# Optimization experiments

Hardware: AMD Instinct MI355X
Metric: run time of the kernel (lower is better)

## Reference

```python
import jax, jax.numpy as jnp
import numpy as np

N, DIM, EDGE_DIM, HEADS, EXP_HEADS, E = 50000, 64, 32, 8, 16, 800000
HEAD_DIM = DIM // HEADS
SCALE = HEAD_DIM ** -0.5
EPS = 1e-16


def setup_inputs() -> dict:
    key = jax.random.key(0)
    ks = jax.random.split(key, 16)
    s = DIM ** -0.5
    return {
        "x": jax.random.normal(ks[0], (N, DIM), jnp.float32),
        "edges": jax.random.normal(ks[1], (E, EDGE_DIM), jnp.float32),
        "edge_index": jax.random.randint(ks[2], (2, E), 0, N, jnp.int64),
        "Wq": jax.random.normal(ks[3], (DIM, DIM), jnp.float32) * s,
        "Wk": jax.random.normal(ks[4], (DIM, DIM), jnp.float32) * s,
        "Wv": jax.random.normal(ks[5], (DIM, DIM), jnp.float32) * s,
        "Wek": jax.random.normal(ks[6], (EDGE_DIM, DIM), jnp.float32) * (EDGE_DIM ** -0.5),
        "Wev": jax.random.normal(ks[7], (EDGE_DIM, DIM), jnp.float32) * (EDGE_DIM ** -0.5),
        "Wexp": jax.random.normal(ks[8], (HEADS, EXP_HEADS), jnp.float32) * (HEADS ** -0.5),
        "Wsq": jax.random.normal(ks[9], (EXP_HEADS, HEADS), jnp.float32) * (EXP_HEADS ** -0.5),
        "bsq": jax.random.normal(ks[10], (HEADS,), jnp.float32) * 0.01,
        "Wout": jax.random.normal(ks[11], (DIM, DIM), jnp.float32) * s,
        "bout": jax.random.normal(ks[12], (DIM,), jnp.float32) * 0.01,
        "temperature": jnp.full((1,), 0.01, jnp.float32),
    }


def reference(x, edges, edge_index, Wq, Wk, Wv, Wek, Wev, Wexp, Wsq, bsq, Wout, bout, temperature):
    n = x.shape[0]
    dst = edge_index[0]  # segment / query index
    src = edge_index[1]  # key/value gather index

    q = (x @ Wq).reshape(n, HEADS, HEAD_DIM)      # [n,h,d]
    k = (x @ Wk).reshape(n, HEADS, HEAD_DIM)
    v = (x @ Wv).reshape(n, HEADS, HEAD_DIM)      # v_non_scatter

    qe = q[dst]                                   # [E,h,d] edge gathers
    ke = k[src]
    ve = v[src]

    edge_k = (edges @ Wek).reshape(-1, HEADS, HEAD_DIM)
    edge_v = (edges @ Wev).reshape(-1, HEADS, HEAD_DIM)

    ke = (ke + edge_k) * SCALE
    attn = jnp.einsum('ehd,ehd->eh', qe, ke) / temperature[0]  # [E,h]
    attn = attn @ Wexp                                          # [E,eh]

    # sparse (segment) softmax over edges grouped by dst, per expanded head
    mx = jax.ops.segment_max(attn, dst, num_segments=n)         # [n,eh]
    ex = jnp.exp(attn - mx[dst])
    sm = jax.ops.segment_sum(ex, dst, num_segments=n)
    attn = ex / (sm[dst] + EPS)

    attn = attn @ Wsq + bsq                                     # [E,h]

    ve = ve + edge_v
    out_e = attn[:, :, None] * ve                               # [E,h,d]
    agg = jax.ops.segment_sum(out_e, dst, num_segments=n)       # [n,h,d]

    out = (v - agg).reshape(n, DIM)                             # graph Laplacian: v - aggregated
    out = out @ Wout + bout
    return out, attn.T  # attention returned as [h, E]
```

## Files before the change

kernel.cpp:

```cpp
#include <hip/hip_runtime.h>
#include <hip/hip_fp16.h>

#define N_NODES 50000
#define DIM 64
#define EDGE_DIM 32
#define HEADS 8
#define EXP_HEADS 16
#define NEDGE 800000
#define SCALE 0.35355339059327373f
#define EPS 1e-16f
#define NEG_BIG -1e30f
#define NB_SCAN ((N_NODES + 255) / 256)

#define RFL(x) __builtin_amdgcn_readfirstlane(x)

__device__ __forceinline__ float h2f(unsigned short u) {
    __half h;
    *reinterpret_cast<unsigned short*>(&h) = u;
    return __half2float(h);
}
__device__ __forceinline__ unsigned short f2h(float f) {
    __half h = __float2half(f);
    return *reinterpret_cast<unsigned short*>(&h);
}

__global__ __launch_bounds__(256) void qkv_kernel(
    const float* __restrict__ x, const float* __restrict__ Wq,
    const float* __restrict__ Wk, const float* __restrict__ Wv,
    float* __restrict__ q, float* __restrict__ k, float* __restrict__ v,
    unsigned short* __restrict__ vh) {
    int gid = blockIdx.x * 256 + threadIdx.x;
    if (gid >= (N_NODES / 4) * DIM) return;
    int quad = gid >> 6, j = gid & 63;
    long i0 = (long)quad * 4;
    float aq[4] = {0,0,0,0}, ak[4] = {0,0,0,0}, av[4] = {0,0,0,0};
#pragma unroll
    for (int l = 0; l < DIM; ++l) {
        float wq = Wq[l * DIM + j], wk = Wk[l * DIM + j], wv = Wv[l * DIM + j];
#pragma unroll
        for (int r = 0; r < 4; ++r) {
            float xv = x[(i0 + r) * DIM + l];
            aq[r] = fmaf(xv, wq, aq[r]);
            ak[r] = fmaf(xv, wk, ak[r]);
            av[r] = fmaf(xv, wv, av[r]);
        }
    }
#pragma unroll
    for (int r = 0; r < 4; ++r) {
        q[(i0 + r) * DIM + j] = aq[r];
        k[(i0 + r) * DIM + j] = ak[r];
        v[(i0 + r) * DIM + j] = av[r];
        vh[(i0 + r) * DIM + j] = f2h(av[r]);
    }
}

__global__ __launch_bounds__(256) void hist_kernel(
    const int* __restrict__ eidx, unsigned* __restrict__ cnt) {
    int e = blockIdx.x * 256 + threadIdx.x;
    if (e >= NEDGE) return;
    atomicAdd(&cnt[eidx[e]], 1u);
}

__global__ __launch_bounds__(256) void scan_reduce(
    const unsigned* __restrict__ cnt, unsigned* __restrict__ blocksum) {
    int gid = blockIdx.x * 256 + threadIdx.x;
    unsigned v = (gid < N_NODES) ? cnt[gid] : 0u;
    v += __shfl_xor(v, 1);  v += __shfl_xor(v, 2);
    v += __shfl_xor(v, 4);  v += __shfl_xor(v, 8);
    v += __shfl_xor(v, 16); v += __shfl_xor(v, 32);
    __shared__ unsigned ws4[4];
    if ((threadIdx.x & 63) == 0) ws4[threadIdx.x >> 6] = v;
    __syncthreads();
    if (threadIdx.x == 0)
        blocksum[blockIdx.x] = ws4[0] + ws4[1] + ws4[2] + ws4[3];
}

__global__ __launch_bounds__(256) void scan_base(
    const unsigned* __restrict__ blocksum, unsigned* __restrict__ blockbase) {
    __shared__ unsigned ps[256];
    int t = threadIdx.x;
    unsigned v = (t < NB_SCAN) ? blocksum[t] : 0u;
    ps[t] = v;
    __syncthreads();
    for (int off = 1; off < 256; off <<= 1) {
        unsigned val = (t >= off) ? ps[t - off] : 0u;
        __syncthreads();
        ps[t] += val;
        __syncthreads();
    }
    blockbase[t] = ps[t] - v;
}

__global__ __launch_bounds__(256) void scan_final(
    const unsigned* __restrict__ cnt, const unsigned* __restrict__ blockbase,
    unsigned* __restrict__ offsets, unsigned* __restrict__ cursor) {
    __shared__ unsigned ps[256];
    int t = threadIdx.x;
    int gid = blockIdx.x * 256 + t;
    unsigned v = (gid < N_NODES) ? cnt[gid] : 0u;
    ps[t] = v;
    __syncthreads();
    for (int off = 1; off < 256; off <<= 1) {
        unsigned val = (t >= off) ? ps[t - off] : 0u;
        __syncthreads();
        ps[t] += val;
        __syncthreads();
    }
    unsigned off_ = blockbase[blockIdx.x] + ps[t] - v;
    if (gid < N_NODES) { offsets[gid] = off_; cursor[gid] = off_; }
    if (gid == N_NODES - 1) offsets[N_NODES] = off_ + v;
}

__global__ __launch_bounds__(256) void scatter_kernel(
    const int* __restrict__ eidx, unsigned* __restrict__ cursor,
    unsigned* __restrict__ perm, unsigned* __restrict__ iperm,
    unsigned* __restrict__ srcs) {
    int e = blockIdx.x * 256 + threadIdx.x;
    if (e >= NEDGE) return;
    int dst = eidx[e];
    unsigned pos = atomicAdd(&cursor[dst], 1u);
    perm[pos] = e;
    iperm[e] = pos;
    srcs[pos] = (unsigned)eidx[NEDGE + e];
}

#define HALVE_BLOCKS 2048
__global__ __launch_bounds__(256) void halve_kernel(
    const float4* __restrict__ src, ushort4* __restrict__ dst) {
    const long n4 = (long)NEDGE * EDGE_DIM / 4;
    long i = (long)blockIdx.x * 256 + threadIdx.x;
    const long stride = (long)HALVE_BLOCKS * 256;
    for (; i < n4; i += stride) {
        float4 t = src[i];
        ushort4 o;
        o.x = f2h(t.x); o.y = f2h(t.y); o.z = f2h(t.z); o.w = f2h(t.w);
        dst[i] = o;
    }
}

__global__ __launch_bounds__(256) void edge_attn_kernel(
    const float* __restrict__ edges,
    const float* __restrict__ q, const float* __restrict__ k,
    const float* __restrict__ Wek,
    const float* __restrict__ temp, const unsigned* __restrict__ perm,
    const unsigned* __restrict__ offsets, const unsigned* __restrict__ srcs,
    float* __restrict__ logit8) {
    int tid = threadIdx.x;
    int w = tid >> 6, lane = tid & 63;
    int h = lane >> 3, d = lane & 7;
    float wekr[4][8];
#pragma unroll
    for (int j = 0; j < 4; ++j)
#pragma unroll
        for (int i = 0; i < 8; ++i)
            wekr[j][i] = Wek[(d * 4 + j) * DIM + h * 8 + i];
    float invt = SCALE / temp[0];
    int n = blockIdx.x * 4 + w;
    unsigned nb = offsets[n];
    int deg = (int)(offsets[n + 1] - nb);
    const float* __restrict__ qp = q + (long)n * DIM;
    float qreg = qp[lane];
    float qv[8];
#pragma unroll
    for (int t = 0; t < 8; ++t) qv[t] = qp[h * 8 + t];
    float g0 = 0.f, g1 = 0.f, g2 = 0.f, g3 = 0.f;
#pragma unroll
    for (int t = 0; t < 8; ++t) {
        g0 = fmaf(qv[t], wekr[0][t], g0);
        g1 = fmaf(qv[t], wekr[1][t], g1);
        g2 = fmaf(qv[t], wekr[2][t], g2);
        g3 = fmaf(qv[t], wekr[3][t], g3);
    }
    int j = 0;
    for (; j + 4 <= deg; j += 4) {
        float p[4];
#pragma unroll
        for (int g2i = 0; g2i < 4; ++g2i) {
            long slot = (long)nb + j + g2i;
            int e_g = RFL((int)perm[slot]);
            int s_g = RFL((int)srcs[slot]);
            float kv = k[(long)s_g * DIM + lane];
            float4 ed = *(const float4*)(edges + (long)e_g * EDGE_DIM + d * 4);
            float pp = qreg * kv;
            pp = fmaf(g0, ed.x, pp);
            pp = fmaf(g1, ed.y, pp);
            pp = fmaf(g2, ed.z, pp);
            pp = fmaf(g3, ed.w, pp);
            p[g2i] = pp;
        }
#pragma unroll
        for (int i = 0; i < 4; ++i) p[i] += __shfl_xor(p[i], 1);
#pragma unroll
        for (int i = 0; i < 4; ++i) p[i] += __shfl_xor(p[i], 2);
#pragma unroll
        for (int i = 0; i < 4; ++i) p[i] += __shfl_xor(p[i], 4);
        if (d == 0) {
#pragma unroll
            for (int i = 0; i < 4; ++i)
                logit8[((long)nb + j + i) * HEADS + h] = p[i] * invt;
        }
    }
    for (; j < deg; ++j) {
        long slot = (long)nb + j;
        int e_g = RFL((int)perm[slot]);
        int s_g = RFL((int)srcs[slot]);
        float kv = k[(long)s_g * DIM + lane];
        float4 ed = *(const float4*)(edges + (long)e_g * EDGE_DIM + d * 4);
        float pp = qreg * kv;
        pp = fmaf(g0, ed.x, pp);
        pp = fmaf(g1, ed.y, pp);
        pp = fmaf(g2, ed.z, pp);
        pp = fmaf(g3, ed.w, pp);
        pp += __shfl_xor(pp, 1);
        pp += __shfl_xor(pp, 2);
        pp += __shfl_xor(pp, 4);
        if (d == 0) logit8[slot * HEADS + h] = pp * invt;
    }
}

__global__ __launch_bounds__(256) void node_fused_kernel(
    const unsigned short* __restrict__ ehalf,
    const unsigned short* __restrict__ vh,
    const float* __restrict__ v, const float* __restrict__ logit8,
    const unsigned* __restrict__ offsets, const unsigned* __restrict__ perm,
    const unsigned* __restrict__ srcs,
    const float* __restrict__ Wexp, const float* __restrict__ Wsq,
    const float* __restrict__ bsq, const float* __restrict__ Wev,
    float* __restrict__ a8s, float* __restrict__ vmagg) {
    int tid = threadIdx.x;
    int w = tid >> 6, lane = tid & 63;
    int g = lane >> 4, t16 = lane & 15;
    int h = lane >> 3, d = lane & 7;
    float we[HEADS];
#pragma unroll
    for (int hh = 0; hh < HEADS; ++hh) we[hh] = Wexp[hh * EXP_HEADS + t16];
    float wsq[HEADS];
#pragma unroll
    for (int j = 0; j < HEADS; ++j) wsq[j] = Wsq[t16 * HEADS + j];
    int hmap = 4 * (t16 & 1) + 2 * ((t16 >> 1) & 1) + ((t16 >> 2) & 1);
    int ih = ((h >> 2) & 1) | (((h >> 1) & 1) << 1) | ((h & 1) << 2);
    float bs_h = bsq[h], bs_w = bsq[hmap];
    bool b0 = (t16 & 1), b1 = (t16 & 2), b2 = (t16 & 4);

    int n = blockIdx.x * 4 + w;
    unsigned nb = offsets[n];
    int deg = (int)(offsets[n + 1] - nb);

    float m = NEG_BIG, s = 0.f;
    for (int j0 = 0; j0 < deg; j0 += 4) {
        const float4* lp = (const float4*)(logit8 + ((long)nb + j0 + g) * HEADS);
        float4 l0 = lp[0], l1 = lp[1];
        float a = l0.x * we[0];
        a = fmaf(l0.y, we[1], a); a = fmaf(l0.z, we[2], a); a = fmaf(l0.w, we[3], a);
        a = fmaf(l1.x, we[4], a); a = fmaf(l1.y, we[5], a);
        a = fmaf(l1.z, we[6], a); a = fmaf(l1.w, we[7], a);
        if (j0 + g < deg) {
            float mn = fmaxf(m, a);
            s = s * __expf(m - mn) + __expf(a - mn);
            m = mn;
        }
    }
#pragma unroll
    for (int off = 16; off < 64; off <<= 1) {
        float m2 = __shfl_xor(m, off), s2 = __shfl_xor(s, off);
        float mn = fmaxf(m, m2);
        s = s * __expf(m - mn) + s2 * __expf(m2 - mn);
        m = mn;
    }
    float rs = 1.f / (s + EPS);

    float acc = 0.f, t0 = 0.f, t1 = 0.f, t2 = 0.f, t3 = 0.f;
    for (int j0 = 0; j0 < deg; j0 += 4) {
        int cnt = deg - j0; if (cnt > 4) cnt = 4;
        const float4* lp = (const float4*)(logit8 + ((long)nb + j0 + g) * HEADS);
        float4 l0 = lp[0], l1 = lp[1];
        float a = l0.x * we[0];
        a = fmaf(l0.y, we[1], a); a = fmaf(l0.z, we[2], a); a = fmaf(l0.w, we[3], a);
        a = fmaf(l1.x, we[4], a); a = fmaf(l1.y, we[5], a);
        a = fmaf(l1.z, we[6], a); a = fmaf(l1.w, we[7], a);
        float p = (g < cnt) ? __expf(a - m) * rs : 0.f;
        float v0 = p * wsq[0], v1 = p * wsq[1], v2 = p * wsq[2], v3 = p * wsq[3];
        float v4 = p * wsq[4], v5 = p * wsq[5], v6 = p * wsq[6], v7 = p * wsq[7];
        float q0, q1, q2, q3, n0, n1, s8;
        q0 = (b0 ? v4 : v0) + __shfl_xor(b0 ? v0 : v4, 1);
        q1 = (b0 ? v5 : v1) + __shfl_xor(b0 ? v1 : v5, 1);
        q2 = (b0 ? v6 : v2) + __shfl_xor(b0 ? v2 : v6, 1);
        q3 = (b0 ? v7 : v3) + __shfl_xor(b0 ? v3 : v7, 1);
        n0 = (b1 ? q2 : q0) + __shfl_xor(b1 ? q0 : q2, 2);
        n1 = (b1 ? q3 : q1) + __shfl_xor(b1 ? q1 : q3, 2);
        s8 = (b2 ? n1 : n0) + __shfl_xor(b2 ? n0 : n1, 4);
        float a8sum = s8 + __shfl_xor(s8, 8);
        if (t16 < 8 && g < cnt)
            a8s[((long)nb + j0 + g) * HEADS + hmap] = a8sum + bs_w;
#pragma unroll
        for (int i = 0; i < 4; ++i) {
            if (i < cnt) {
                long slot = (long)nb + j0 + i;
                int e_g = RFL((int)perm[slot]);
                int s_g = RFL((int)srcs[slot]);
                float a8 = __shfl(a8sum, i * 16 + ih) + bs_h;
                float vv = h2f(vh[(long)s_g * DIM + lane]);
                ushort4 ue = *(const ushort4*)(ehalf + (long)e_g * EDGE_DIM + d * 4);
                acc = fmaf(a8, vv, acc);
                t0 = fmaf(a8, h2f(ue.x), t0);
                t1 = fmaf(a8, h2f(ue.y), t1);
                t2 = fmaf(a8, h2f(ue.z), t2);
                t3 = fmaf(a8, h2f(ue.w), t3);
            }
        }
    }
    float ev = 0.f;
#pragma unroll
    for (int l = 0; l < EDGE_DIM; ++l) {
        float tv = ((l & 3) == 0) ? t0 : ((l & 3) == 1) ? t1 : ((l & 3) == 2) ? t2 : t3;
        float tl = __shfl(tv, h * 8 + (l >> 2));
        ev = fmaf(tl, Wev[l * DIM + lane], ev);
    }
    vmagg[(long)n * DIM + lane] = v[(long)n * DIM + lane] - (acc + ev);
}

__global__ __launch_bounds__(256) void transpose_kernel(
    const float* __restrict__ a8s, const unsigned* __restrict__ iperm,
    float* __restrict__ out2) {
    int e = blockIdx.x * 256 + threadIdx.x;
    if (e >= NEDGE) return;
    long sj = iperm[e];
    const float4* p = (const float4*)(a8s + sj * HEADS);
    float4 lo = p[0], hi = p[1];
    out2[0L * NEDGE + e] = lo.x; out2[1L * NEDGE + e] = lo.y;
    out2[2L * NEDGE + e] = lo.z; out2[3L * NEDGE + e] = lo.w;
    out2[4L * NEDGE + e] = hi.x; out2[5L * NEDGE + e] = hi.y;
    out2[6L * NEDGE + e] = hi.z; out2[7L * NEDGE + e] = hi.w;
}

__global__ __launch_bounds__(256) void out_kernel(
    const float* __restrict__ vmagg, const float* __restrict__ Wout,
    const float* __restrict__ bout, float* __restrict__ out) {
    int gid = blockIdx.x * 256 + threadIdx.x;
    if (gid >= (N_NODES / 4) * DIM) return;
    int quad = gid >> 6, j = gid & 63;
    long i0 = (long)quad * 4;
    float b = bout[j];
    float ac[4] = {b, b, b, b};
#pragma unroll
    for (int l = 0; l < DIM; ++l) {
        float wv = Wout[l * DIM + j];
#pragma unroll
        for (int r = 0; r < 4; ++r)
            ac[r] = fmaf(vmagg[(i0 + r) * DIM + l], wv, ac[r]);
    }
#pragma unroll
    for (int r = 0; r < 4; ++r) out[(i0 + r) * DIM + j] = ac[r];
}

extern "C" void kernel_launch(void* const* d_in, const int* in_sizes, int n_in,
                              void* d_out, int out_size, void* d_ws, size_t ws_size,
                              hipStream_t stream) {
    const float* x     = (const float*)d_in[0];
    const float* edges = (const float*)d_in[1];
    const int*   eidx  = (const int*)d_in[2];
    const float* Wq    = (const float*)d_in[3];
    const float* Wk    = (const float*)d_in[4];
    const float* Wv    = (const float*)d_in[5];
    const float* Wek   = (const float*)d_in[6];
    const float* Wev   = (const float*)d_in[7];
    const float* Wexp  = (const float*)d_in[8];
    const float* Wsq   = (const float*)d_in[9];
    const float* bsq   = (const float*)d_in[10];
    const float* Wout  = (const float*)d_in[11];
    const float* bout  = (const float*)d_in[12];
    const float* temp  = (const float*)d_in[13];

    float* ws = (float*)d_ws;
    float* q       = ws;
    float* k       = ws + 3200000L;
    float* v       = ws + 6400000L;
    float* logit8  = ws + 9600000L;
    float* vmagg   = ws + 16000000L;
    float* a8s     = q;
    unsigned* perm      = (unsigned*)(ws + 19200000L);
    unsigned* iperm     = perm + NEDGE;
    unsigned* srcs      = iperm + NEDGE;
    unsigned* cnt       = srcs + NEDGE;
    unsigned* offsets   = cnt + N_NODES;
    unsigned* cursor    = offsets + N_NODES + 1;
    unsigned* blocksum  = cursor + N_NODES;
    unsigned* blockbase = blocksum + 256;
    unsigned short* ehalf = (unsigned short*)(ws + 21800000L);
    unsigned short* vh    = (unsigned short*)(ws + 34600000L);

    hipMemsetAsync(cnt, 0, (size_t)N_NODES * sizeof(unsigned), stream);

    float* out1 = (float*)d_out;
    float* out2 = out1 + (long)N_NODES * DIM;

    qkv_kernel<<<(N_NODES / 4 * DIM + 255) / 256, 256, 0, stream>>>(x, Wq, Wk, Wv, q, k, v, vh);
    hist_kernel<<<(NEDGE + 255) / 256, 256, 0, stream>>>(eidx, cnt);
    scan_reduce<<<NB_SCAN, 256, 0, stream>>>(cnt, blocksum);
    scan_base<<<1, 256, 0, stream>>>(blocksum, blockbase);
    scan_final<<<NB_SCAN, 256, 0, stream>>>(cnt, blockbase, offsets, cursor);
    halve_kernel<<<HALVE_BLOCKS, 256, 0, stream>>>((const float4*)edges, (ushort4*)ehalf);
    scatter_kernel<<<(NEDGE + 255) / 256, 256, 0, stream>>>(eidx, cursor, perm, iperm, srcs);
    edge_attn_kernel<<<N_NODES / 4, 256, 0, stream>>>(edges, q, k, Wek, temp,
                                                      perm, offsets, srcs, logit8);
    node_fused_kernel<<<N_NODES / 4, 256, 0, stream>>>(ehalf, vh, v, logit8, offsets, perm, srcs,
                                                       Wexp, Wsq, bsq, Wev, a8s, vmagg);
    transpose_kernel<<<(NEDGE + 255) / 256, 256, 0, stream>>>(a8s, iperm, out2);
    out_kernel<<<(N_NODES / 4 * DIM + 255) / 256, 256, 0, stream>>>(vmagg, Wout, bout, out1);
}
```

Before: 466.4 us.

## Read fp16 keys and edges in edge attention; unroll node softmax loops by eight

```diff
diff --git a/kernel.cpp b/kernel.cpp
--- a/kernel.cpp
+++ b/kernel.cpp
@@ -27,8 +27,8 @@
 __global__ __launch_bounds__(256) void qkv_kernel(
     const float* __restrict__ x, const float* __restrict__ Wq,
     const float* __restrict__ Wk, const float* __restrict__ Wv,
-    float* __restrict__ q, float* __restrict__ k, float* __restrict__ v,
-    unsigned short* __restrict__ vh) {
+    float* __restrict__ q, unsigned short* __restrict__ kh,
+    float* __restrict__ v, unsigned short* __restrict__ vh) {
     int gid = blockIdx.x * 256 + threadIdx.x;
     if (gid >= (N_NODES / 4) * DIM) return;
     int quad = gid >> 6, j = gid & 63;
@@ -48,7 +48,7 @@
 #pragma unroll
     for (int r = 0; r < 4; ++r) {
         q[(i0 + r) * DIM + j] = aq[r];
-        k[(i0 + r) * DIM + j] = ak[r];
+        kh[(i0 + r) * DIM + j] = f2h(ak[r]);
         v[(i0 + r) * DIM + j] = av[r];
         vh[(i0 + r) * DIM + j] = f2h(av[r]);
     }
@@ -139,8 +139,8 @@
 }
 
 __global__ __launch_bounds__(256) void edge_attn_kernel(
-    const float* __restrict__ edges,
-    const float* __restrict__ q, const float* __restrict__ k,
+    const unsigned short* __restrict__ ehalf,
+    const float* __restrict__ q, const unsigned short* __restrict__ kh,
     const float* __restrict__ Wek,
     const float* __restrict__ temp, const unsigned* __restrict__ perm,
     const unsigned* __restrict__ offsets, const unsigned* __restrict__ srcs,
@@ -179,13 +179,13 @@
             long slot = (long)nb + j + g2i;
             int e_g = RFL((int)perm[slot]);
             int s_g = RFL((int)srcs[slot]);
-            float kv = k[(long)s_g * DIM + lane];
-            float4 ed = *(const float4*)(edges + (long)e_g * EDGE_DIM + d * 4);
+            float kv = h2f(kh[(long)s_g * DIM + lane]);
+            ushort4 ue = *(const ushort4*)(ehalf + (long)e_g * EDGE_DIM + d * 4);
             float pp = qreg * kv;
-            pp = fmaf(g0, ed.x, pp);
-            pp = fmaf(g1, ed.y, pp);
-            pp = fmaf(g2, ed.z, pp);
-            pp = fmaf(g3, ed.w, pp);
+            pp = fmaf(g0, h2f(ue.x), pp);
+            pp = fmaf(g1, h2f(ue.y), pp);
+            pp = fmaf(g2, h2f(ue.z), pp);
+            pp = fmaf(g3, h2f(ue.w), pp);
             p[g2i] = pp;
         }
 #pragma unroll
@@ -204,13 +204,13 @@
         long slot = (long)nb + j;
         int e_g = RFL((int)perm[slot]);
         int s_g = RFL((int)srcs[slot]);
-        float kv = k[(long)s_g * DIM + lane];
-        float4 ed = *(const float4*)(edges + (long)e_g * EDGE_DIM + d * 4);
+        float kv = h2f(kh[(long)s_g * DIM + lane]);
+        ushort4 ue = *(const ushort4*)(ehalf + (long)e_g * EDGE_DIM + d * 4);
         float pp = qreg * kv;
-        pp = fmaf(g0, ed.x, pp);
-        pp = fmaf(g1, ed.y, pp);
-        pp = fmaf(g2, ed.z, pp);
-        pp = fmaf(g3, ed.w, pp);
+        pp = fmaf(g0, h2f(ue.x), pp);
+        pp = fmaf(g1, h2f(ue.y), pp);
+        pp = fmaf(g2, h2f(ue.z), pp);
+        pp = fmaf(g3, h2f(ue.w), pp);
         pp += __shfl_xor(pp, 1);
         pp += __shfl_xor(pp, 2);
         pp += __shfl_xor(pp, 4);
@@ -246,8 +246,28 @@
     unsigned nb = offsets[n];
     int deg = (int)(offsets[n + 1] - nb);
 
-    float m = NEG_BIG, s = 0.f;
-    for (int j0 = 0; j0 < deg; j0 += 4) {
+    float ma = NEG_BIG, sa = 0.f, mb = NEG_BIG, sb = 0.f;
+    int j0 = 0;
+    for (; j0 + 8 <= deg; j0 += 8) {
+        const float4* lpA = (const float4*)(logit8 + ((long)nb + j0 + g) * HEADS);
+        const float4* lpB = (const float4*)(logit8 + ((long)nb + j0 + 4 + g) * HEADS);
+        float4 a0 = lpA[0], a1 = lpA[1], c0 = lpB[0], c1 = lpB[1];
+        float aA = a0.x * we[0];
+        float aB = c0.x * we[0];
+        aA = fmaf(a0.y, we[1], aA); aB = fmaf(c0.y, we[1], aB);
+        aA = fmaf(a0.z, we[2], aA); aB = fmaf(c0.z, we[2], aB);
+        aA = fmaf(a0.w, we[3], aA); aB = fmaf(c0.w, we[3], aB);
+        aA = fmaf(a1.x, we[4], aA); aB = fmaf(c1.x, we[4], aB);
+        aA = fmaf(a1.y, we[5], aA); aB = fmaf(c1.y, we[5], aB);
+        aA = fmaf(a1.z, we[6], aA); aB = fmaf(c1.z, we[6], aB);
+        aA = fmaf(a1.w, we[7], aA); aB = fmaf(c1.w, we[7], aB);
+        float mnA = fmaxf(ma, aA);
+        float mnB = fmaxf(mb, aB);
+        sa = sa * __expf(ma - mnA) + __expf(aA - mnA);
+        sb = sb * __expf(mb - mnB) + __expf(aB - mnB);
+        ma = mnA; mb = mnB;
+    }
+    for (; j0 < deg; j0 += 4) {
         const float4* lp = (const float4*)(logit8 + ((long)nb + j0 + g) * HEADS);
         float4 l0 = lp[0], l1 = lp[1];
         float a = l0.x * we[0];
@@ -255,11 +275,17 @@
         a = fmaf(l1.x, we[4], a); a = fmaf(l1.y, we[5], a);
         a = fmaf(l1.z, we[6], a); a = fmaf(l1.w, we[7], a);
         if (j0 + g < deg) {
-            float mn = fmaxf(m, a);
-            s = s * __expf(m - mn) + __expf(a - mn);
-            m = mn;
-        }
-    }
+            float mn = fmaxf(ma, a);
+            sa = sa * __expf(ma - mn) + __expf(a - mn);
+            ma = mn;
+        }
+    }
+    {
+        float mn = fmaxf(ma, mb);
+        sa = sa * __expf(ma - mn) + sb * __expf(mb - mn);
+        ma = mn;
+    }
+    float m = ma, s = sa;
 #pragma unroll
     for (int off = 16; off < 64; off <<= 1) {
         float m2 = __shfl_xor(m, off), s2 = __shfl_xor(s, off);
@@ -270,7 +296,78 @@
     float rs = 1.f / (s + EPS);
 
     float acc = 0.f, t0 = 0.f, t1 = 0.f, t2 = 0.f, t3 = 0.f;
-    for (int j0 = 0; j0 < deg; j0 += 4) {
+    j0 = 0;
+    for (; j0 + 8 <= deg; j0 += 8) {
+        const float4* lpA = (const float4*)(logit8 + ((long)nb + j0 + g) * HEADS);
+        const float4* lpB = (const float4*)(logit8 + ((long)nb + j0 + 4 + g) * HEADS);
+        float4 a0 = lpA[0], a1 = lpA[1], c0 = lpB[0], c1 = lpB[1];
+        float aA = a0.x * we[0];
+        float aB = c0.x * we[0];
+        aA = fmaf(a0.y, we[1], aA); aB = fmaf(c0.y, we[1], aB);
+        aA = fmaf(a0.z, we[2], aA); aB = fmaf(c0.z, we[2], aB);
+        aA = fmaf(a0.w, we[3], aA); aB = fmaf(c0.w, we[3], aB);
+        aA = fmaf(a1.x, we[4], aA); aB = fmaf(c1.x, we[4], aB);
+        aA = fmaf(a1.y, we[5], aA); aB = fmaf(c1.y, we[5], aB);
+        aA = fmaf(a1.z, we[6], aA); aB = fmaf(c1.z, we[6], aB);
+        aA = fmaf(a1.w, we[7], aA); aB = fmaf(c1.w, we[7], aB);
+        float pA = __expf(aA - m) * rs;
+        float pB = __expf(aB - m) * rs;
+        float vA0 = pA * wsq[0], vA1 = pA * wsq[1], vA2 = pA * wsq[2], vA3 = pA * wsq[3];
+        float vA4 = pA * wsq[4], vA5 = pA * wsq[5], vA6 = pA * wsq[6], vA7 = pA * wsq[7];
+        float vB0 = pB * wsq[0], vB1 = pB * wsq[1], vB2 = pB * wsq[2], vB3 = pB * wsq[3];
+        float vB4 = pB * wsq[4], vB5 = pB * wsq[5], vB6 = pB * wsq[6], vB7 = pB * wsq[7];
+        float qA0, qA1, qA2, qA3, nA0, nA1, sA8;
+        float qB0, qB1, qB2, qB3, nB0, nB1, sB8;
+        qA0 = (b0 ? vA4 : vA0) + __shfl_xor(b0 ? vA0 : vA4, 1);
+        qB0 = (b0 ? vB4 : vB0) + __shfl_xor(b0 ? vB0 : vB4, 1);
+        qA1 = (b0 ? vA5 : vA1) + __shfl_xor(b0 ? vA1 : vA5, 1);
+        qB1 = (b0 ? vB5 : vB1) + __shfl_xor(b0 ? vB1 : vB5, 1);
+        qA2 = (b0 ? vA6 : vA2) + __shfl_xor(b0 ? vA2 : vA6, 1);
+        qB2 = (b0 ? vB6 : vB2) + __shfl_xor(b0 ? vB2 : vB6, 1);
+        qA3 = (b0 ? vA7 : vA3) + __shfl_xor(b0 ? vA3 : vA7, 1);
+        qB3 = (b0 ? vB7 : vB3) + __shfl_xor(b0 ? vB3 : vB7, 1);
+        nA0 = (b1 ? qA2 : qA0) + __shfl_xor(b1 ? qA0 : qA2, 2);
+        nB0 = (b1 ? qB2 : qB0) + __shfl_xor(b1 ? qB0 : qB2, 2);
+        nA1 = (b1 ? qA3 : qA1) + __shfl_xor(b1 ? qA1 : qA3, 2);
+        nB1 = (b1 ? qB3 : qB1) + __shfl_xor(b1 ? qB1 : qB3, 2);
+        sA8 = (b2 ? nA1 : nA0) + __shfl_xor(b2 ? nA0 : nA1, 4);
+        sB8 = (b2 ? nB1 : nB0) + __shfl_xor(b2 ? nB0 : nB1, 4);
+        float a8sumA = sA8 + __shfl_xor(sA8, 8);
+        float a8sumB = sB8 + __shfl_xor(sB8, 8);
+        if (t16 < 8) {
+            a8s[((long)nb + j0 + g) * HEADS + hmap] = a8sumA + bs_w;
+            a8s[((long)nb + j0 + 4 + g) * HEADS + hmap] = a8sumB + bs_w;
+        }
+#pragma unroll
+        for (int i = 0; i < 4; ++i) {
+            long slot = (long)nb + j0 + i;
+            int e_g = RFL((int)perm[slot]);
+            int s_g = RFL((int)srcs[slot]);
+            float a8 = __shfl(a8sumA, i * 16 + ih) + bs_h;
+            float vv = h2f(vh[(long)s_g * DIM + lane]);
+            ushort4 ue = *(const ushort4*)(ehalf + (long)e_g * EDGE_DIM + d * 4);
+            acc = fmaf(a8, vv, acc);
+            t0 = fmaf(a8, h2f(ue.x), t0);
+            t1 = fmaf(a8, h2f(ue.y), t1);
+            t2 = fmaf(a8, h2f(ue.z), t2);
+            t3 = fmaf(a8, h2f(ue.w), t3);
+        }
+#pragma unroll
+        for (int i = 0; i < 4; ++i) {
+            long slot = (long)nb + j0 + 4 + i;
+            int e_g = RFL((int)perm[slot]);
+            int s_g = RFL((int)srcs[slot]);
+            float a8 = __shfl(a8sumB, i * 16 + ih) + bs_h;
+            float vv = h2f(vh[(long)s_g * DIM + lane]);
+            ushort4 ue = *(const ushort4*)(ehalf + (long)e_g * EDGE_DIM + d * 4);
+            acc = fmaf(a8, vv, acc);
+            t0 = fmaf(a8, h2f(ue.x), t0);
+            t1 = fmaf(a8, h2f(ue.y), t1);
+            t2 = fmaf(a8, h2f(ue.z), t2);
+            t3 = fmaf(a8, h2f(ue.w), t3);
+        }
+    }
+    for (; j0 < deg; j0 += 4) {
         int cnt = deg - j0; if (cnt > 4) cnt = 4;
         const float4* lp = (const float4*)(logit8 + ((long)nb + j0 + g) * HEADS);
         float4 l0 = lp[0], l1 = lp[1];
@@ -373,7 +470,7 @@
 
     float* ws = (float*)d_ws;
     float* q       = ws;
-    float* k       = ws + 3200000L;
+    unsigned short* kh = (unsigned short*)(ws + 3200000L);
     float* v       = ws + 6400000L;
     float* logit8  = ws + 9600000L;
     float* vmagg   = ws + 16000000L;
@@ -394,14 +491,14 @@
     float* out1 = (float*)d_out;
     float* out2 = out1 + (long)N_NODES * DIM;
 
-    qkv_kernel<<<(N_NODES / 4 * DIM + 255) / 256, 256, 0, stream>>>(x, Wq, Wk, Wv, q, k, v, vh);
+    qkv_kernel<<<(N_NODES / 4 * DIM + 255) / 256, 256, 0, stream>>>(x, Wq, Wk, Wv, q, kh, v, vh);
     hist_kernel<<<(NEDGE + 255) / 256, 256, 0, stream>>>(eidx, cnt);
     scan_reduce<<<NB_SCAN, 256, 0, stream>>>(cnt, blocksum);
     scan_base<<<1, 256, 0, stream>>>(blocksum, blockbase);
     scan_final<<<NB_SCAN, 256, 0, stream>>>(cnt, blockbase, offsets, cursor);
     halve_kernel<<<HALVE_BLOCKS, 256, 0, stream>>>((const float4*)edges, (ushort4*)ehalf);
     scatter_kernel<<<(NEDGE + 255) / 256, 256, 0, stream>>>(eidx, cursor, perm, iperm, srcs);
-    edge_attn_kernel<<<N_NODES / 4, 256, 0, stream>>>(edges, q, k, Wek, temp,
+    edge_attn_kernel<<<N_NODES / 4, 256, 0, stream>>>(ehalf, q, kh, Wek, temp,
                                                       perm, offsets, srcs, logit8);
     node_fused_kernel<<<N_NODES / 4, 256, 0, stream>>>(ehalf, vh, v, logit8, offsets, perm, srcs,
                                                        Wexp, Wsq, bsq, Wev, a8s, vmagg);
```

New measurement: 460.9 us. Within noise of the previous version (-1.2%).

## Use fp16 keys and edges in attention kernel and batch gathers ahead of math

Applied to the files above, without the earlier changes.

```diff
diff --git a/kernel.cpp b/kernel.cpp
--- a/kernel.cpp
+++ b/kernel.cpp
@@ -27,8 +27,8 @@
 __global__ __launch_bounds__(256) void qkv_kernel(
     const float* __restrict__ x, const float* __restrict__ Wq,
     const float* __restrict__ Wk, const float* __restrict__ Wv,
-    float* __restrict__ q, float* __restrict__ k, float* __restrict__ v,
-    unsigned short* __restrict__ vh) {
+    float* __restrict__ q, unsigned short* __restrict__ kh,
+    float* __restrict__ v, unsigned short* __restrict__ vh) {
     int gid = blockIdx.x * 256 + threadIdx.x;
     if (gid >= (N_NODES / 4) * DIM) return;
     int quad = gid >> 6, j = gid & 63;
@@ -48,7 +48,7 @@
 #pragma unroll
     for (int r = 0; r < 4; ++r) {
         q[(i0 + r) * DIM + j] = aq[r];
-        k[(i0 + r) * DIM + j] = ak[r];
+        kh[(i0 + r) * DIM + j] = f2h(ak[r]);
         v[(i0 + r) * DIM + j] = av[r];
         vh[(i0 + r) * DIM + j] = f2h(av[r]);
     }
@@ -139,8 +139,8 @@
 }
 
 __global__ __launch_bounds__(256) void edge_attn_kernel(
-    const float* __restrict__ edges,
-    const float* __restrict__ q, const float* __restrict__ k,
+    const unsigned short* __restrict__ ehalf,
+    const float* __restrict__ q, const unsigned short* __restrict__ kh,
     const float* __restrict__ Wek,
     const float* __restrict__ temp, const unsigned* __restrict__ perm,
     const unsigned* __restrict__ offsets, const unsigned* __restrict__ srcs,
@@ -173,20 +173,24 @@
     }
     int j = 0;
     for (; j + 4 <= deg; j += 4) {
-        float p[4];
-#pragma unroll
-        for (int g2i = 0; g2i < 4; ++g2i) {
-            long slot = (long)nb + j + g2i;
+        unsigned short rk[4]; ushort4 re[4];
+#pragma unroll
+        for (int i = 0; i < 4; ++i) {
+            long slot = (long)nb + j + i;
             int e_g = RFL((int)perm[slot]);
             int s_g = RFL((int)srcs[slot]);
-            float kv = k[(long)s_g * DIM + lane];
-            float4 ed = *(const float4*)(edges + (long)e_g * EDGE_DIM + d * 4);
-            float pp = qreg * kv;
-            pp = fmaf(g0, ed.x, pp);
-            pp = fmaf(g1, ed.y, pp);
-            pp = fmaf(g2, ed.z, pp);
-            pp = fmaf(g3, ed.w, pp);
-            p[g2i] = pp;
+            rk[i] = kh[(long)s_g * DIM + lane];
+            re[i] = *(const ushort4*)(ehalf + (long)e_g * EDGE_DIM + d * 4);
+        }
+        float p[4];
+#pragma unroll
+        for (int i = 0; i < 4; ++i) {
+            float pp = qreg * h2f(rk[i]);
+            pp = fmaf(g0, h2f(re[i].x), pp);
+            pp = fmaf(g1, h2f(re[i].y), pp);
+            pp = fmaf(g2, h2f(re[i].z), pp);
+            pp = fmaf(g3, h2f(re[i].w), pp);
+            p[i] = pp;
         }
 #pragma unroll
         for (int i = 0; i < 4; ++i) p[i] += __shfl_xor(p[i], 1);
@@ -204,13 +208,13 @@
         long slot = (long)nb + j;
         int e_g = RFL((int)perm[slot]);
         int s_g = RFL((int)srcs[slot]);
-        float kv = k[(long)s_g * DIM + lane];
-        float4 ed = *(const float4*)(edges + (long)e_g * EDGE_DIM + d * 4);
+        float kv = h2f(kh[(long)s_g * DIM + lane]);
+        ushort4 ue = *(const ushort4*)(ehalf + (long)e_g * EDGE_DIM + d * 4);
         float pp = qreg * kv;
-        pp = fmaf(g0, ed.x, pp);
-        pp = fmaf(g1, ed.y, pp);
-        pp = fmaf(g2, ed.z, pp);
-        pp = fmaf(g3, ed.w, pp);
+        pp = fmaf(g0, h2f(ue.x), pp);
+        pp = fmaf(g1, h2f(ue.y), pp);
+        pp = fmaf(g2, h2f(ue.z), pp);
+        pp = fmaf(g3, h2f(ue.w), pp);
         pp += __shfl_xor(pp, 1);
         pp += __shfl_xor(pp, 2);
         pp += __shfl_xor(pp, 4);
@@ -269,11 +273,22 @@
     }
     float rs = 1.f / (s + EPS);
 
-    float acc = 0.f, t0 = 0.f, t1 = 0.f, t2 = 0.f, t3 = 0.f;
+    float accA = 0.f, accB = 0.f, t0 = 0.f, t1 = 0.f, t2 = 0.f, t3 = 0.f;
     for (int j0 = 0; j0 < deg; j0 += 4) {
         int cnt = deg - j0; if (cnt > 4) cnt = 4;
         const float4* lp = (const float4*)(logit8 + ((long)nb + j0 + g) * HEADS);
         float4 l0 = lp[0], l1 = lp[1];
+        unsigned short rv[4]; ushort4 re[4];
+#pragma unroll
+        for (int i = 0; i < 4; ++i) {
+            if (i < cnt) {
+                long slot = (long)nb + j0 + i;
+                int e_g = RFL((int)perm[slot]);
+                int s_g = RFL((int)srcs[slot]);
+                rv[i] = vh[(long)s_g * DIM + lane];
+                re[i] = *(const ushort4*)(ehalf + (long)e_g * EDGE_DIM + d * 4);
+            }
+        }
         float a = l0.x * we[0];
         a = fmaf(l0.y, we[1], a); a = fmaf(l0.z, we[2], a); a = fmaf(l0.w, we[3], a);
         a = fmaf(l1.x, we[4], a); a = fmaf(l1.y, we[5], a);
@@ -295,20 +310,18 @@
 #pragma unroll
         for (int i = 0; i < 4; ++i) {
             if (i < cnt) {
-                long slot = (long)nb + j0 + i;
-                int e_g = RFL((int)perm[slot]);
-                int s_g = RFL((int)srcs[slot]);
                 float a8 = __shfl(a8sum, i * 16 + ih) + bs_h;
-                float vv = h2f(vh[(long)s_g * DIM + lane]);
-                ushort4 ue = *(const ushort4*)(ehalf + (long)e_g * EDGE_DIM + d * 4);
-                acc = fmaf(a8, vv, acc);
-                t0 = fmaf(a8, h2f(ue.x), t0);
-                t1 = fmaf(a8, h2f(ue.y), t1);
-                t2 = fmaf(a8, h2f(ue.z), t2);
-                t3 = fmaf(a8, h2f(ue.w), t3);
+                float vv = h2f(rv[i]);
+                if (i & 1) accB = fmaf(a8, vv, accB);
+                else       accA = fmaf(a8, vv, accA);
+                t0 = fmaf(a8, h2f(re[i].x), t0);
+                t1 = fmaf(a8, h2f(re[i].y), t1);
+                t2 = fmaf(a8, h2f(re[i].z), t2);
+                t3 = fmaf(a8, h2f(re[i].w), t3);
             }
         }
     }
+    float acc = accA + accB;
     float ev = 0.f;
 #pragma unroll
     for (int l = 0; l < EDGE_DIM; ++l) {
@@ -373,7 +386,7 @@
 
     float* ws = (float*)d_ws;
     float* q       = ws;
-    float* k       = ws + 3200000L;
+    unsigned short* kh = (unsigned short*)(ws + 3200000L);
     float* v       = ws + 6400000L;
     float* logit8  = ws + 9600000L;
     float* vmagg   = ws + 16000000L;
@@ -394,14 +407,14 @@
     float* out1 = (float*)d_out;
     float* out2 = out1 + (long)N_NODES * DIM;
 
-    qkv_kernel<<<(N_NODES / 4 * DIM + 255) / 256, 256, 0, stream>>>(x, Wq, Wk, Wv, q, k, v, vh);
+    qkv_kernel<<<(N_NODES / 4 * DIM + 255) / 256, 256, 0, stream>>>(x, Wq, Wk, Wv, q, kh, v, vh);
     hist_kernel<<<(NEDGE + 255) / 256, 256, 0, stream>>>(eidx, cnt);
     scan_reduce<<<NB_SCAN, 256, 0, stream>>>(cnt, blocksum);
     scan_base<<<1, 256, 0, stream>>>(blocksum, blockbase);
     scan_final<<<NB_SCAN, 256, 0, stream>>>(cnt, blockbase, offsets, cursor);
     halve_kernel<<<HALVE_BLOCKS, 256, 0, stream>>>((const float4*)edges, (ushort4*)ehalf);
     scatter_kernel<<<(NEDGE + 255) / 256, 256, 0, stream>>>(eidx, cursor, perm, iperm, srcs);
-    edge_attn_kernel<<<N_NODES / 4, 256, 0, stream>>>(edges, q, k, Wek, temp,
+    edge_attn_kernel<<<N_NODES / 4, 256, 0, stream>>>(ehalf, q, kh, Wek, temp,
                                                       perm, offsets, srcs, logit8);
     node_fused_kernel<<<N_NODES / 4, 256, 0, stream>>>(ehalf, vh, v, logit8, offsets, perm, srcs,
                                                        Wexp, Wsq, bsq, Wev, a8s, vmagg);
```

Measured after the change: 486.1 us. +4.2%, slower.

## Pre-permute edge features into dst-sorted fp16 layout during scatter; store k as fp16

Applied to the files above, without the earlier changes.

```diff
diff --git a/kernel.cpp b/kernel.cpp
--- a/kernel.cpp
+++ b/kernel.cpp
@@ -27,8 +27,8 @@
 __global__ __launch_bounds__(256) void qkv_kernel(
     const float* __restrict__ x, const float* __restrict__ Wq,
     const float* __restrict__ Wk, const float* __restrict__ Wv,
-    float* __restrict__ q, float* __restrict__ k, float* __restrict__ v,
-    unsigned short* __restrict__ vh) {
+    float* __restrict__ q, unsigned short* __restrict__ kh,
+    float* __restrict__ v, unsigned short* __restrict__ vh) {
     int gid = blockIdx.x * 256 + threadIdx.x;
     if (gid >= (N_NODES / 4) * DIM) return;
     int quad = gid >> 6, j = gid & 63;
@@ -48,7 +48,7 @@
 #pragma unroll
     for (int r = 0; r < 4; ++r) {
         q[(i0 + r) * DIM + j] = aq[r];
-        k[(i0 + r) * DIM + j] = ak[r];
+        kh[(i0 + r) * DIM + j] = f2h(ak[r]);
         v[(i0 + r) * DIM + j] = av[r];
         vh[(i0 + r) * DIM + j] = f2h(av[r]);
     }
@@ -112,37 +112,32 @@
 }
 
 __global__ __launch_bounds__(256) void scatter_kernel(
-    const int* __restrict__ eidx, unsigned* __restrict__ cursor,
-    unsigned* __restrict__ perm, unsigned* __restrict__ iperm,
-    unsigned* __restrict__ srcs) {
+    const int* __restrict__ eidx, const float4* __restrict__ edges4,
+    unsigned* __restrict__ cursor,
+    unsigned* __restrict__ iperm, unsigned* __restrict__ srcs,
+    unsigned short* __restrict__ esort) {
     int e = blockIdx.x * 256 + threadIdx.x;
     if (e >= NEDGE) return;
     int dst = eidx[e];
     unsigned pos = atomicAdd(&cursor[dst], 1u);
-    perm[pos] = e;
     iperm[e] = pos;
     srcs[pos] = (unsigned)eidx[NEDGE + e];
-}
-
-#define HALVE_BLOCKS 2048
-__global__ __launch_bounds__(256) void halve_kernel(
-    const float4* __restrict__ src, ushort4* __restrict__ dst) {
-    const long n4 = (long)NEDGE * EDGE_DIM / 4;
-    long i = (long)blockIdx.x * 256 + threadIdx.x;
-    const long stride = (long)HALVE_BLOCKS * 256;
-    for (; i < n4; i += stride) {
+    const float4* src = edges4 + (long)e * 8;
+    ushort4* dst4 = (ushort4*)(esort + (long)pos * EDGE_DIM);
+#pragma unroll
+    for (int i = 0; i < 8; ++i) {
         float4 t = src[i];
         ushort4 o;
         o.x = f2h(t.x); o.y = f2h(t.y); o.z = f2h(t.z); o.w = f2h(t.w);
-        dst[i] = o;
+        dst4[i] = o;
     }
 }
 
 __global__ __launch_bounds__(256) void edge_attn_kernel(
-    const float* __restrict__ edges,
-    const float* __restrict__ q, const float* __restrict__ k,
+    const unsigned short* __restrict__ esort,
+    const float* __restrict__ q, const unsigned short* __restrict__ kh,
     const float* __restrict__ Wek,
-    const float* __restrict__ temp, const unsigned* __restrict__ perm,
+    const float* __restrict__ temp,
     const unsigned* __restrict__ offsets, const unsigned* __restrict__ srcs,
     float* __restrict__ logit8) {
     int tid = threadIdx.x;
@@ -177,15 +172,14 @@
 #pragma unroll
         for (int g2i = 0; g2i < 4; ++g2i) {
             long slot = (long)nb + j + g2i;
-            int e_g = RFL((int)perm[slot]);
             int s_g = RFL((int)srcs[slot]);
-            float kv = k[(long)s_g * DIM + lane];
-            float4 ed = *(const float4*)(edges + (long)e_g * EDGE_DIM + d * 4);
+            float kv = h2f(kh[(long)s_g * DIM + lane]);
+            ushort4 ue = *(const ushort4*)(esort + slot * EDGE_DIM + d * 4);
             float pp = qreg * kv;
-            pp = fmaf(g0, ed.x, pp);
-            pp = fmaf(g1, ed.y, pp);
-            pp = fmaf(g2, ed.z, pp);
-            pp = fmaf(g3, ed.w, pp);
+            pp = fmaf(g0, h2f(ue.x), pp);
+            pp = fmaf(g1, h2f(ue.y), pp);
+            pp = fmaf(g2, h2f(ue.z), pp);
+            pp = fmaf(g3, h2f(ue.w), pp);
             p[g2i] = pp;
         }
 #pragma unroll
@@ -202,15 +196,14 @@
     }
     for (; j < deg; ++j) {
         long slot = (long)nb + j;
-        int e_g = RFL((int)perm[slot]);
         int s_g = RFL((int)srcs[slot]);
-        float kv = k[(long)s_g * DIM + lane];
-        float4 ed = *(const float4*)(edges + (long)e_g * EDGE_DIM + d * 4);
+        float kv = h2f(kh[(long)s_g * DIM + lane]);
+        ushort4 ue = *(const ushort4*)(esort + slot * EDGE_DIM + d * 4);
         float pp = qreg * kv;
-        pp = fmaf(g0, ed.x, pp);
-        pp = fmaf(g1, ed.y, pp);
-        pp = fmaf(g2, ed.z, pp);
-        pp = fmaf(g3, ed.w, pp);
+        pp = fmaf(g0, h2f(ue.x), pp);
+        pp = fmaf(g1, h2f(ue.y), pp);
+        pp = fmaf(g2, h2f(ue.z), pp);
+        pp = fmaf(g3, h2f(ue.w), pp);
         pp += __shfl_xor(pp, 1);
         pp += __shfl_xor(pp, 2);
         pp += __shfl_xor(pp, 4);
@@ -219,10 +212,10 @@
 }
 
 __global__ __launch_bounds__(256) void node_fused_kernel(
-    const unsigned short* __restrict__ ehalf,
+    const unsigned short* __restrict__ esort,
     const unsigned short* __restrict__ vh,
     const float* __restrict__ v, const float* __restrict__ logit8,
-    const unsigned* __restrict__ offsets, const unsigned* __restrict__ perm,
+    const unsigned* __restrict__ offsets,
     const unsigned* __restrict__ srcs,
     const float* __restrict__ Wexp, const float* __restrict__ Wsq,
     const float* __restrict__ bsq, const float* __restrict__ Wev,
@@ -296,11 +289,10 @@
         for (int i = 0; i < 4; ++i) {
             if (i < cnt) {
                 long slot = (long)nb + j0 + i;
-                int e_g = RFL((int)perm[slot]);
                 int s_g = RFL((int)srcs[slot]);
                 float a8 = __shfl(a8sum, i * 16 + ih) + bs_h;
                 float vv = h2f(vh[(long)s_g * DIM + lane]);
-                ushort4 ue = *(const ushort4*)(ehalf + (long)e_g * EDGE_DIM + d * 4);
+                ushort4 ue = *(const ushort4*)(esort + slot * EDGE_DIM + d * 4);
                 acc = fmaf(a8, vv, acc);
                 t0 = fmaf(a8, h2f(ue.x), t0);
                 t1 = fmaf(a8, h2f(ue.y), t1);
@@ -373,20 +365,19 @@
 
     float* ws = (float*)d_ws;
     float* q       = ws;
-    float* k       = ws + 3200000L;
+    unsigned short* kh = (unsigned short*)(ws + 3200000L);
     float* v       = ws + 6400000L;
     float* logit8  = ws + 9600000L;
     float* vmagg   = ws + 16000000L;
     float* a8s     = q;
-    unsigned* perm      = (unsigned*)(ws + 19200000L);
-    unsigned* iperm     = perm + NEDGE;
+    unsigned* iperm     = (unsigned*)(ws + 19200000L);
     unsigned* srcs      = iperm + NEDGE;
     unsigned* cnt       = srcs + NEDGE;
     unsigned* offsets   = cnt + N_NODES;
     unsigned* cursor    = offsets + N_NODES + 1;
     unsigned* blocksum  = cursor + N_NODES;
     unsigned* blockbase = blocksum + 256;
-    unsigned short* ehalf = (unsigned short*)(ws + 21800000L);
+    unsigned short* esort = (unsigned short*)(ws + 21800000L);
     unsigned short* vh    = (unsigned short*)(ws + 34600000L);
 
     hipMemsetAsync(cnt, 0, (size_t)N_NODES * sizeof(unsigned), stream);
@@ -394,16 +385,16 @@
     float* out1 = (float*)d_out;
     float* out2 = out1 + (long)N_NODES * DIM;
 
-    qkv_kernel<<<(N_NODES / 4 * DIM + 255) / 256, 256, 0, stream>>>(x, Wq, Wk, Wv, q, k, v, vh);
+    qkv_kernel<<<(N_NODES / 4 * DIM + 255) / 256, 256, 0, stream>>>(x, Wq, Wk, Wv, q, kh, v, vh);
     hist_kernel<<<(NEDGE + 255) / 256, 256, 0, stream>>>(eidx, cnt);
     scan_reduce<<<NB_SCAN, 256, 0, stream>>>(cnt, blocksum);
     scan_base<<<1, 256, 0, stream>>>(blocksum, blockbase);
     scan_final<<<NB_SCAN, 256, 0, stream>>>(cnt, blockbase, offsets, cursor);
-    halve_kernel<<<HALVE_BLOCKS, 256, 0, stream>>>((const float4*)edges, (ushort4*)ehalf);
-    scatter_kernel<<<(NEDGE + 255) / 256, 256, 0, stream>>>(eidx, cursor, perm, iperm, srcs);
-    edge_attn_kernel<<<N_NODES / 4, 256, 0, stream>>>(edges, q, k, Wek, temp,
-                                                      perm, offsets, srcs, logit8);
-    node_fused_kernel<<<N_NODES / 4, 256, 0, stream>>>(ehalf, vh, v, logit8, offsets, perm, srcs,
+    scatter_kernel<<<(NEDGE + 255) / 256, 256, 0, stream>>>(eidx, (const float4*)edges,
+                                                            cursor, iperm, srcs, esort);
+    edge_attn_kernel<<<N_NODES / 4, 256, 0, stream>>>(esort, q, kh, Wek, temp,
+                                                      offsets, srcs, logit8);
+    node_fused_kernel<<<N_NODES / 4, 256, 0, stream>>>(esort, vh, v, logit8, offsets, srcs,
                                                        Wexp, Wsq, bsq, Wev, a8s, vmagg);
     transpose_kernel<<<(NEDGE + 255) / 256, 256, 0, stream>>>(a8s, iperm, out2);
     out_kernel<<<(N_NODES / 4 * DIM + 255) / 256, 256, 0, stream>>>(vmagg, Wout, bout, out1);
```

After: 437.4 us, median of 2. 1.07x faster.
